# Kernel optimization log

Hardware: AMD Instinct MI355X
Metric: run time of the kernel (lower is better)

## Reference

```python
import jax, jax.numpy as jnp
import numpy as np

INPUT_DIM = 256
N_CLASSES = 100
MAX_DEPTH = 12
N_NODES = 2 ** MAX_DEPTH - 1   # 4095 internal nodes
N_LEAVES = 2 ** MAX_DEPTH      # 4096 leaves


def setup_inputs() -> dict:
    key = jax.random.key(0)
    k_x, k_sf, k_st, k_lp = jax.random.split(key, 4)
    x = jax.random.normal(k_x, (500000, INPUT_DIM), dtype=jnp.float32)
    # split_features ~ U[0, input_dim)  (torch.rand * input_dim)
    split_features = jax.random.uniform(k_sf, (N_NODES,), dtype=jnp.float32) * INPUT_DIM
    split_thresholds = jax.random.normal(k_st, (N_NODES,), dtype=jnp.float32) / np.sqrt(INPUT_DIM)
    # xavier_uniform with gain 1/sqrt(n_classes): bound = gain*sqrt(6/(fan_in+fan_out))
    bound = (1.0 / np.sqrt(N_CLASSES)) * np.sqrt(6.0 / (N_LEAVES + N_CLASSES))
    leaf_probabilities = jax.random.uniform(
        k_lp, (N_LEAVES, N_CLASSES), dtype=jnp.float32, minval=-bound, maxval=bound)
    return {"x": x, "split_features": split_features,
            "split_thresholds": split_thresholds,
            "leaf_probabilities": leaf_probabilities}


def reference(x, split_features, split_thresholds, leaf_probabilities):
    batch = x.shape[0]
    # per-node feature index: floor then clamp to [0, input_dim-1]
    node_features = jnp.clip(jnp.floor(split_features), 0, INPUT_DIM - 1).astype(jnp.int32)
    node_idx = jnp.zeros((batch,), dtype=jnp.int32)
    for _ in range(MAX_DEPTH):  # fixed small unrolled traversal
        feats = node_features[node_idx]                       # [B]
        thr = split_thresholds[node_idx]                      # [B]
        vals = jnp.take_along_axis(x, feats[:, None], axis=1)[:, 0]  # [B]
        node_idx = node_idx * 2 + 1 + (vals > thr).astype(jnp.int32)
    leaf_idx = node_idx - N_NODES                             # [B] in [0, N_LEAVES)
    return jax.nn.softmax(leaf_probabilities[leaf_idx], axis=1)
```

## Files before the change

kernel.cpp:

```cpp
#include <hip/hip_runtime.h>
#include <math.h>

#define INPUT_DIM 256
#define N_CLASSES 100
#define MAX_DEPTH 12
#define N_NODES   4095
#define N_LEAVES  4096

#define TPB   512
#define NWAVE 8
#define RPW   5
#define DEPTH 3
#define ROWP  260
#define NF4   (N_CLASSES / 4)
#define NBLK  256

#define WAITV(N) asm volatile("s_waitcnt vmcnt(" #N ")" ::: "memory")
#define SCHEDB() __builtin_amdgcn_sched_barrier(0)

typedef float f32x4 __attribute__((ext_vector_type(4)));

__device__ __forceinline__ void async_load16(const void* gsrc, void* ldst) {
    __builtin_amdgcn_global_load_lds(
        (const __attribute__((address_space(1))) unsigned int*)gsrc,
        (__attribute__((address_space(3))) unsigned int*)ldst, 16, 0, 0);
}

__global__ __launch_bounds__(64) void softmax_rows_kernel(
    const float* __restrict__ lp, float* __restrict__ tab) {
    const int row  = blockIdx.x;
    const int lane = threadIdx.x;
    const float* src = lp + (size_t)row * N_CLASSES;

    float v0 = src[lane];
    float v1 = (lane + 64 < N_CLASSES) ? src[lane + 64] : -INFINITY;

    float m = fmaxf(v0, v1);
    #pragma unroll
    for (int off = 32; off > 0; off >>= 1) m = fmaxf(m, __shfl_xor(m, off));

    float e0 = expf(v0 - m);
    float e1 = (lane + 64 < N_CLASSES) ? expf(v1 - m) : 0.0f;
    float s = e0 + e1;
    #pragma unroll
    for (int off = 32; off > 0; off >>= 1) s += __shfl_xor(s, off);

    const float inv = 1.0f / s;
    tab[(size_t)row * N_CLASSES + lane] = e0 * inv;
    if (lane + 64 < N_CLASSES)
        tab[(size_t)row * N_CLASSES + lane + 64] = e1 * inv;
}

__global__ __launch_bounds__(TPB) void tree_stream_kernel(
    const float* __restrict__ x,
    const float* __restrict__ split_features,
    const float* __restrict__ split_thresholds,
    const f32x4* __restrict__ tab4,
    f32x4* __restrict__ out4,
    int batch, int nunits) {
    __shared__ float         s_rows[NWAVE][DEPTH][RPW][ROWP];
    __shared__ float         s_thr[N_NODES];
    __shared__ unsigned char s_feat[N_NODES + 1];

    const int tid  = threadIdx.x;
    const int wid  = tid >> 6;
    const int lane = tid & 63;

    for (int i = tid; i < N_NODES; i += TPB) {
        s_thr[i] = split_thresholds[i];
        int f = (int)floorf(split_features[i]);
        s_feat[i] = (unsigned char)min(max(f, 0), INPUT_DIM - 1);
    }
    __syncthreads();

    const int NPIPE = gridDim.x * NWAVE;
    const int W     = blockIdx.x * NWAVE + wid;

    auto stage = [&](int k, int slot) {
        long g = (long)W + (long)k * NPIPE;
        if (g >= nunits) g = nunits - 1;
        const size_t rbase = (size_t)g * RPW;
        #pragma unroll
        for (int j = 0; j < RPW; ++j) {
            const float* src = x + (rbase + j) * INPUT_DIM + lane * 4;
            async_load16((const void*)src, (void*)&s_rows[wid][slot][j][0]);
        }
    };

    stage(0, 0);
    stage(1, 1);

    for (int k = 0; ; ++k) {
        const long g = (long)W + (long)k * NPIPE;
        if (g >= nunits) break;

        stage(k + 2, (k + 2) % 3);
        SCHEDB();
        if (k == 0)      WAITV(10);
        else if (k == 1) WAITV(14);
        else             WAITV(18);
        SCHEDB();

        int leaf = 0;
        if (lane < RPW) {
            const float* row = &s_rows[wid][k % 3][lane][0];
            float t = s_thr[0];
            int   f = s_feat[0];
            int   n = 0;
            #pragma unroll
            for (int d = 0; d < MAX_DEPTH; ++d) {
                const int l = 2 * n + 1;
                if (d < MAX_DEPTH - 1) {
                    const float tl = s_thr[l],  tr = s_thr[l + 1];
                    const int   fl = s_feat[l], fr = s_feat[l + 1];
                    const int go = row[f] > t ? 1 : 0;
                    t = go ? tr : tl;
                    f = go ? fr : fl;
                    n = l + go;
                } else {
                    n = l + (row[f] > t ? 1 : 0);
                }
            }
            leaf = n - N_NODES;
        }

        const size_t base4 = (size_t)g * (RPW * NF4);
        const long   rem   = (long)batch * NF4 - (long)base4;
        const int    maxj  = rem < RPW * NF4 ? (int)rem : RPW * NF4;
        #pragma unroll
        for (int t2 = 0; t2 < 2; ++t2) {
            const int j = lane + t2 * 64;
            if (j < maxj) {
                const int r = j / NF4;
                const int q = j - r * NF4;
                const int lf = __shfl(leaf, r);
                f32x4 v = tab4[(size_t)lf * NF4 + q];
                __builtin_nontemporal_store(v, &out4[base4 + j]);
            }
        }
    }
}

__global__ __launch_bounds__(256) void fused_kernel(
    const float* __restrict__ x,
    const float* __restrict__ split_features,
    const float* __restrict__ split_thresholds,
    const float* __restrict__ lp,
    float* __restrict__ out, int batch) {
    __shared__ float2 s_nodes[N_NODES];
    for (int i = threadIdx.x; i < N_NODES; i += blockDim.x) {
        int f = (int)floorf(split_features[i]);
        f = min(max(f, 0), INPUT_DIM - 1);
        float2 n; n.x = split_thresholds[i]; n.y = __int_as_float(f);
        s_nodes[i] = n;
    }
    __syncthreads();

    const int b = blockIdx.x * blockDim.x + threadIdx.x;
    if (b >= batch) return;

    const float* row = x + (size_t)b * INPUT_DIM;
    int node = 0;
    #pragma unroll
    for (int d = 0; d < MAX_DEPTH; ++d) {
        const float2 n = s_nodes[node];
        const float val = row[__float_as_int(n.y)];
        node = 2 * node + 1 + (val > n.x ? 1 : 0);
    }
    const int leaf = node - N_NODES;

    const float* src = lp + (size_t)leaf * N_CLASSES;
    float m = -INFINITY;
    for (int cidx = 0; cidx < N_CLASSES; ++cidx) m = fmaxf(m, src[cidx]);
    float s = 0.0f;
    float e[N_CLASSES];
    for (int cidx = 0; cidx < N_CLASSES; ++cidx) { e[cidx] = expf(src[cidx] - m); s += e[cidx]; }
    const float inv = 1.0f / s;
    float* dst = out + (size_t)b * N_CLASSES;
    for (int cidx = 0; cidx < N_CLASSES; ++cidx) dst[cidx] = e[cidx] * inv;
}

extern "C" void kernel_launch(void* const* d_in, const int* in_sizes, int n_in,
                              void* d_out, int out_size, void* d_ws, size_t ws_size,
                              hipStream_t stream) {
    const float* x  = (const float*)d_in[0];
    const float* sf = (const float*)d_in[1];
    const float* st = (const float*)d_in[2];
    const float* lp = (const float*)d_in[3];
    float* out = (float*)d_out;

    const int batch = in_sizes[0] / INPUT_DIM;

    const size_t tab_bytes = (size_t)N_LEAVES * N_CLASSES * sizeof(float);

    if (ws_size >= tab_bytes && batch > 0) {
        float* tab = (float*)d_ws;

        softmax_rows_kernel<<<N_LEAVES, 64, 0, stream>>>(lp, tab);

        const int nunits = (batch + RPW - 1) / RPW;
        int nblk = (nunits + NWAVE - 1) / NWAVE;
        if (nblk > NBLK) nblk = NBLK;
        tree_stream_kernel<<<nblk, TPB, 0, stream>>>(
            x, sf, st, (const f32x4*)tab, (f32x4*)out, batch, nunits);
    } else {
        fused_kernel<<<(batch + 255) / 256, 256, 0, stream>>>(
            x, sf, st, lp, out, batch);
    }
}
```

Baseline: 153.9 us.

## Split tree traversal and output gather into separate kernels via leaf index buffer

Traversal now only streams x rows and writes a 16-bit leaf index per sample to workspace. A separate grid-stride kernel gathers softmaxed table rows into the output. This separates the read-heavy and write-heavy phases so each can run at full bandwidth, and it shortens the vmcnt waits because output stores no longer sit in the traversal's memory queue. The cost is an extra launch, a small leaf buffer round trip, and losing the overlap between reading x and writing output. Row loads are also clamped to batch-1 for tail safety.

```diff
diff --git a/kernel.cpp b/kernel.cpp
--- a/kernel.cpp
+++ b/kernel.cpp
@@ -51,12 +51,11 @@
         tab[(size_t)row * N_CLASSES + lane + 64] = e1 * inv;
 }
 
-__global__ __launch_bounds__(TPB) void tree_stream_kernel(
+__global__ __launch_bounds__(TPB) void traverse_kernel(
     const float* __restrict__ x,
     const float* __restrict__ split_features,
     const float* __restrict__ split_thresholds,
-    const f32x4* __restrict__ tab4,
-    f32x4* __restrict__ out4,
+    unsigned short* __restrict__ leaf_out,
     int batch, int nunits) {
     __shared__ float         s_rows[NWAVE][DEPTH][RPW][ROWP];
     __shared__ float         s_thr[N_NODES];
@@ -79,10 +78,11 @@
     auto stage = [&](int k, int slot) {
         long g = (long)W + (long)k * NPIPE;
         if (g >= nunits) g = nunits - 1;
-        const size_t rbase = (size_t)g * RPW;
         #pragma unroll
         for (int j = 0; j < RPW; ++j) {
-            const float* src = x + (rbase + j) * INPUT_DIM + lane * 4;
+            long r = g * RPW + j;
+            if (r >= batch) r = batch - 1;
+            const float* src = x + (size_t)r * INPUT_DIM + lane * 4;
             async_load16((const void*)src, (void*)&s_rows[wid][slot][j][0]);
         }
     };
@@ -97,11 +97,10 @@
         stage(k + 2, (k + 2) % 3);
         SCHEDB();
         if (k == 0)      WAITV(10);
-        else if (k == 1) WAITV(14);
-        else             WAITV(18);
+        else if (k == 1) WAITV(11);
+        else             WAITV(12);
         SCHEDB();
 
-        int leaf = 0;
         if (lane < RPW) {
             const float* row = &s_rows[wid][k % 3][lane][0];
             float t = s_thr[0];
@@ -121,23 +120,24 @@
                     n = l + (row[f] > t ? 1 : 0);
                 }
             }
-            leaf = n - N_NODES;
+            const long s = g * RPW + lane;
+            if (s < batch)
+                leaf_out[s] = (unsigned short)(n - N_NODES);
         }
-
-        const size_t base4 = (size_t)g * (RPW * NF4);
-        const long   rem   = (long)batch * NF4 - (long)base4;
-        const int    maxj  = rem < RPW * NF4 ? (int)rem : RPW * NF4;
-        #pragma unroll
-        for (int t2 = 0; t2 < 2; ++t2) {
-            const int j = lane + t2 * 64;
-            if (j < maxj) {
-                const int r = j / NF4;
-                const int q = j - r * NF4;
-                const int lf = __shfl(leaf, r);
-                f32x4 v = tab4[(size_t)lf * NF4 + q];
-                __builtin_nontemporal_store(v, &out4[base4 + j]);
-            }
-        }
+    }
+}
+
+__global__ __launch_bounds__(256) void gather_out_kernel(
+    const f32x4* __restrict__ tab4,
+    const unsigned short* __restrict__ leaf,
+    f32x4* __restrict__ out4, int total4) {
+    for (int j = blockIdx.x * 256 + threadIdx.x; j < total4;
+         j += gridDim.x * 256) {
+        const int r = j / NF4;
+        const int q = j - r * NF4;
+        const int lf = leaf[r];
+        f32x4 v = tab4[(size_t)lf * NF4 + q];
+        __builtin_nontemporal_store(v, &out4[j]);
     }
 }
 
@@ -192,17 +192,25 @@
     const int batch = in_sizes[0] / INPUT_DIM;
 
     const size_t tab_bytes = (size_t)N_LEAVES * N_CLASSES * sizeof(float);
-
-    if (ws_size >= tab_bytes && batch > 0) {
+    const size_t need = tab_bytes + (size_t)batch * sizeof(unsigned short);
+
+    if (ws_size >= need && batch > 0) {
         float* tab = (float*)d_ws;
+        unsigned short* leaf = (unsigned short*)((char*)d_ws + tab_bytes);
 
         softmax_rows_kernel<<<N_LEAVES, 64, 0, stream>>>(lp, tab);
 
         const int nunits = (batch + RPW - 1) / RPW;
         int nblk = (nunits + NWAVE - 1) / NWAVE;
         if (nblk > NBLK) nblk = NBLK;
-        tree_stream_kernel<<<nblk, TPB, 0, stream>>>(
-            x, sf, st, (const f32x4*)tab, (f32x4*)out, batch, nunits);
+        traverse_kernel<<<nblk, TPB, 0, stream>>>(
+            x, sf, st, leaf, batch, nunits);
+
+        const int total4 = batch * NF4;
+        int nb2 = (total4 + 255) / 256;
+        if (nb2 > 2048) nb2 = 2048;
+        gather_out_kernel<<<nb2, 256, 0, stream>>>(
+            (const f32x4*)tab, leaf, (f32x4*)out, total4);
     } else {
         fused_kernel<<<(batch + 255) / 256, 256, 0, stream>>>(
             x, sf, st, lp, out, batch);
```

Result: faster. 140.2 us (-8.9%).

## Split tree kernel into producer traversal waves and consumer output-writer waves

Applied to the files above, without the earlier changes.

Restructures the streaming kernel into warp specialization: six waves per block prefetch x rows asynchronously into LDS and traverse the tree, publishing leaf indices into an LDS ring buffer, while two waves each serve three producers by gathering softmax table rows and writing output. The handoff uses LDS ready/done counters with sleep-polling. This is meant to overlap the large output write stream with input loads and traversal instead of serializing them inside each wave. It adds spin-wait synchronization overhead and leaves fewer waves issuing input loads, and the 2 writer waves must sustain all of the output bandwidth.

```diff
diff --git a/kernel.cpp b/kernel.cpp
--- a/kernel.cpp
+++ b/kernel.cpp
@@ -9,13 +9,18 @@
 
 #define TPB   512
 #define NWAVE 8
+#define PPB   6
+#define CPB   2
 #define RPW   5
-#define DEPTH 3
+#define TBUF  3
+#define DEPTHQ 8
 #define ROWP  260
 #define NF4   (N_CLASSES / 4)
+#define UF4   (RPW * NF4)
 #define NBLK  256
 
 #define WAITV(N) asm volatile("s_waitcnt vmcnt(" #N ")" ::: "memory")
+#define WAITLGKM() asm volatile("s_waitcnt lgkmcnt(0)" ::: "memory")
 #define SCHEDB() __builtin_amdgcn_sched_barrier(0)
 
 typedef float f32x4 __attribute__((ext_vector_type(4)));
@@ -51,16 +56,19 @@
         tab[(size_t)row * N_CLASSES + lane + 64] = e1 * inv;
 }
 
-__global__ __launch_bounds__(TPB) void tree_stream_kernel(
+__global__ __launch_bounds__(TPB) void tree_pc_kernel(
     const float* __restrict__ x,
     const float* __restrict__ split_features,
     const float* __restrict__ split_thresholds,
     const f32x4* __restrict__ tab4,
     f32x4* __restrict__ out4,
     int batch, int nunits) {
-    __shared__ float         s_rows[NWAVE][DEPTH][RPW][ROWP];
-    __shared__ float         s_thr[N_NODES];
-    __shared__ unsigned char s_feat[N_NODES + 1];
+    __shared__ float          s_rows[PPB][TBUF][RPW][ROWP];
+    __shared__ float          s_thr[N_NODES];
+    __shared__ unsigned char  s_feat[N_NODES + 1];
+    __shared__ unsigned short s_ring[PPB][DEPTHQ][RPW + 3];
+    __shared__ unsigned int   s_ready[PPB];
+    __shared__ unsigned int   s_done[PPB];
 
     const int tid  = threadIdx.x;
     const int wid  = tid >> 6;
@@ -71,71 +79,112 @@
         int f = (int)floorf(split_features[i]);
         s_feat[i] = (unsigned char)min(max(f, 0), INPUT_DIM - 1);
     }
+    if (tid < PPB) { s_ready[tid] = 0u; s_done[tid] = 0u; }
     __syncthreads();
 
-    const int NPIPE = gridDim.x * NWAVE;
-    const int W     = blockIdx.x * NWAVE + wid;
-
-    auto stage = [&](int k, int slot) {
-        long g = (long)W + (long)k * NPIPE;
-        if (g >= nunits) g = nunits - 1;
-        const size_t rbase = (size_t)g * RPW;
+    const int NP = gridDim.x * PPB;
+    const int total4 = batch * NF4;
+
+    if (wid < PPB) {
+        const int P  = blockIdx.x * PPB + wid;
+        const int nk = (P < nunits) ? ((nunits - 1 - P) / NP + 1) : 0;
+        volatile unsigned int* vdone = &s_done[wid];
+
+        auto stage = [&](int k, int slot) {
+            long g = (long)P + (long)k * NP;
+            if (g >= nunits) g = nunits - 1;
+            #pragma unroll
+            for (int j = 0; j < RPW; ++j) {
+                long r = g * RPW + j;
+                if (r >= batch) r = batch - 1;
+                const float* src = x + (size_t)r * INPUT_DIM + lane * 4;
+                async_load16((const void*)src, (void*)&s_rows[wid][slot][j][0]);
+            }
+        };
+
+        if (nk > 0) { stage(0, 0); stage(1, 1); }
+
+        for (int k = 0; k < nk; ++k) {
+            stage(k + 2, (k + 2) % TBUF);
+            SCHEDB();
+            WAITV(10);
+            SCHEDB();
+
+            int leafv = 0;
+            if (lane < RPW) {
+                const float* row = &s_rows[wid][k % TBUF][lane][0];
+                float t = s_thr[0];
+                int   f = s_feat[0];
+                int   n = 0;
+                #pragma unroll
+                for (int d = 0; d < MAX_DEPTH; ++d) {
+                    const int l = 2 * n + 1;
+                    if (d < MAX_DEPTH - 1) {
+                        const float tl = s_thr[l],  tr = s_thr[l + 1];
+                        const int   fl = s_feat[l], fr = s_feat[l + 1];
+                        const int go = row[f] > t ? 1 : 0;
+                        t = go ? tr : tl;
+                        f = go ? fr : fl;
+                        n = l + go;
+                    } else {
+                        n = l + (row[f] > t ? 1 : 0);
+                    }
+                }
+                leafv = n - N_NODES;
+            }
+
+            while ((int)*vdone < k - DEPTHQ + 1) __builtin_amdgcn_s_sleep(1);
+            if (lane < RPW)
+                s_ring[wid][k % DEPTHQ][lane] = (unsigned short)leafv;
+            WAITLGKM();
+            if (lane == 0)
+                *(volatile unsigned int*)&s_ready[wid] = (unsigned int)(k + 1);
+        }
+        WAITV(0);
+    } else {
+        const int c = wid - PPB;
+        const int j0 = lane;
+        const int j1 = lane + 64;
+        const int r0 = j0 / NF4,             q0 = j0 - r0 * NF4;
+        const int r1c = j1 < UF4 ? j1 / NF4 : RPW - 1;
+        const int q1 = j1 - (j1 / NF4) * NF4;
+
+        int nk_[3]; int kmax = 0;
         #pragma unroll
-        for (int j = 0; j < RPW; ++j) {
-            const float* src = x + (rbase + j) * INPUT_DIM + lane * 4;
-            async_load16((const void*)src, (void*)&s_rows[wid][slot][j][0]);
+        for (int i = 0; i < 3; ++i) {
+            const int pl = 3 * c + i;
+            const int P  = blockIdx.x * PPB + pl;
+            nk_[i] = (P < nunits) ? ((nunits - 1 - P) / NP + 1) : 0;
+            kmax = max(kmax, nk_[i]);
         }
-    };
-
-    stage(0, 0);
-    stage(1, 1);
-
-    for (int k = 0; ; ++k) {
-        const long g = (long)W + (long)k * NPIPE;
-        if (g >= nunits) break;
-
-        stage(k + 2, (k + 2) % 3);
-        SCHEDB();
-        if (k == 0)      WAITV(10);
-        else if (k == 1) WAITV(14);
-        else             WAITV(18);
-        SCHEDB();
-
-        int leaf = 0;
-        if (lane < RPW) {
-            const float* row = &s_rows[wid][k % 3][lane][0];
-            float t = s_thr[0];
-            int   f = s_feat[0];
-            int   n = 0;
+
+        for (int k = 0; k < kmax; ++k) {
             #pragma unroll
-            for (int d = 0; d < MAX_DEPTH; ++d) {
-                const int l = 2 * n + 1;
-                if (d < MAX_DEPTH - 1) {
-                    const float tl = s_thr[l],  tr = s_thr[l + 1];
-                    const int   fl = s_feat[l], fr = s_feat[l + 1];
-                    const int go = row[f] > t ? 1 : 0;
-                    t = go ? tr : tl;
-                    f = go ? fr : fl;
-                    n = l + go;
-                } else {
-                    n = l + (row[f] > t ? 1 : 0);
+            for (int i = 0; i < 3; ++i) {
+                if (k >= nk_[i]) continue;
+                const int pl = 3 * c + i;
+                const long g = (long)(blockIdx.x * PPB + pl) + (long)k * NP;
+
+                volatile unsigned int* vready = &s_ready[pl];
+                while ((int)*vready < k + 1) __builtin_amdgcn_s_sleep(1);
+
+                const int slot = k % DEPTHQ;
+                const int lf0 = s_ring[pl][slot][r0];
+                const int lf1 = s_ring[pl][slot][r1c];
+                WAITLGKM();
+                if (lane == 0)
+                    *(volatile unsigned int*)&s_done[pl] = (unsigned int)(k + 1);
+
+                const long base4 = g * UF4;
+                const int  maxj  = (int)min((long)UF4, (long)total4 - base4);
+                if (j0 < maxj) {
+                    f32x4 v = tab4[(size_t)lf0 * NF4 + q0];
+                    __builtin_nontemporal_store(v, &out4[base4 + j0]);
                 }
-            }
-            leaf = n - N_NODES;
-        }
-
-        const size_t base4 = (size_t)g * (RPW * NF4);
-        const long   rem   = (long)batch * NF4 - (long)base4;
-        const int    maxj  = rem < RPW * NF4 ? (int)rem : RPW * NF4;
-        #pragma unroll
-        for (int t2 = 0; t2 < 2; ++t2) {
-            const int j = lane + t2 * 64;
-            if (j < maxj) {
-                const int r = j / NF4;
-                const int q = j - r * NF4;
-                const int lf = __shfl(leaf, r);
-                f32x4 v = tab4[(size_t)lf * NF4 + q];
-                __builtin_nontemporal_store(v, &out4[base4 + j]);
+                if (j1 < maxj) {
+                    f32x4 v = tab4[(size_t)lf1 * NF4 + q1];
+                    __builtin_nontemporal_store(v, &out4[base4 + j1]);
+                }
             }
         }
     }
@@ -193,15 +242,15 @@
 
     const size_t tab_bytes = (size_t)N_LEAVES * N_CLASSES * sizeof(float);
 
-    if (ws_size >= tab_bytes && batch > 0) {
+    if (ws_size >= tab_bytes && batch >= 4096) {
         float* tab = (float*)d_ws;
 
         softmax_rows_kernel<<<N_LEAVES, 64, 0, stream>>>(lp, tab);
 
         const int nunits = (batch + RPW - 1) / RPW;
-        int nblk = (nunits + NWAVE - 1) / NWAVE;
+        int nblk = (nunits + PPB - 1) / PPB;
         if (nblk > NBLK) nblk = NBLK;
-        tree_stream_kernel<<<nblk, TPB, 0, stream>>>(
+        tree_pc_kernel<<<nblk, TPB, 0, stream>>>(
             x, sf, st, (const f32x4*)tab, (f32x4*)out, batch, nunits);
     } else {
         fused_kernel<<<(batch + 255) / 256, 256, 0, stream>>>(
```

After: 237.4 us. +54.2%, slower.
